# Kernel optimization log

Measured on AMD Instinct MI355X. Metric: run time of the kernel, lower is better.

The kernel has to match this reference:

```python
import jax, jax.numpy as jnp
import numpy as np

B, T, D, H = 2, 2048, 1024, 16
DK = D // H


def setup_inputs() -> dict:
    key = jax.random.key(0)
    ks = jax.random.split(key, 12)
    s = 0.02
    return {
        "query": jax.random.normal(ks[0], (B, T, D), jnp.float32),
        "key": jax.random.normal(ks[1], (B, T, D), jnp.float32),
        "value": jax.random.normal(ks[2], (B, T, D), jnp.float32),
        "mask": jax.random.randint(ks[3], (B, T), 0, 2) != 0,  # True = keep
        "Wq": jax.random.normal(ks[4], (D, D), jnp.float32) * s,
        "bq": jnp.zeros((D,), jnp.float32),
        "Wk": jax.random.normal(ks[5], (D, D), jnp.float32) * s,
        "bk": jnp.zeros((D,), jnp.float32),
        "Wv": jax.random.normal(ks[6], (D, D), jnp.float32) * s,
        "bv": jnp.zeros((D,), jnp.float32),
        "Wo": jax.random.normal(ks[7], (D, D), jnp.float32) * s,
        "bo": jnp.zeros((D,), jnp.float32),
    }


def _split_heads(x):
    # [B, S, D] -> [B, H, S, DK]
    b, s, _ = x.shape
    return x.reshape(b, s, H, DK).transpose(0, 2, 1, 3)


def reference(query, key, value, mask, Wq, bq, Wk, bk, Wv, bv, Wo, bo):
    # torch Linear: y = x @ W.T + b
    q = _split_heads(query @ Wq.T + bq)   # [B,H,T,DK]
    k = _split_heads(key @ Wk.T + bk)     # [B,H,S,DK]
    v = _split_heads(value @ Wv.T + bv)   # [B,H,S,DK]
    scale = 1.0 / np.sqrt(DK).astype(np.float32)
    scores = jnp.einsum('bhtd,bhsd->bhts', q, k) * scale  # [B,H,T,S]
    # key-padding mask [B,S] -> broadcast [B,1,1,S], True = keep
    scores = jnp.where(mask[:, None, None, :], scores, -jnp.inf)
    attn = jax.nn.softmax(scores, axis=-1)
    out = jnp.einsum('bhts,bhsd->bhtd', attn, v)           # [B,H,T,DK]
    out = out.transpose(0, 2, 1, 3).reshape(query.shape[0], -1, D)
    return out @ Wo.T + bo
```

## Files before the change

### kernel.cpp

```cpp
#include <hip/hip_runtime.h>
#include <stdint.h>

#define B_SZ 2
#define T_SEQ 2048
#define DMODEL 1024
#define NHEAD 16
#define DKH 64
#define M_ROWS (B_SZ * T_SEQ)

#define LDT 72

#define INP_E  4194304u
#define W_E    1048576u

typedef __bf16 bf16x8 __attribute__((ext_vector_type(8)));
typedef float  f32x4  __attribute__((ext_vector_type(4)));

__device__ __forceinline__ unsigned short f2bf(float f) {
    unsigned u = __builtin_bit_cast(unsigned, f);
    u += 0x7fffu + ((u >> 16) & 1u);
    return (unsigned short)(u >> 16);
}
__device__ __forceinline__ uint4 cvt8(const float* p) {
    float4 f0 = *(const float4*)p, f1 = *(const float4*)(p + 4);
    uint4 r;
    r.x = (unsigned)f2bf(f0.x) | ((unsigned)f2bf(f0.y) << 16);
    r.y = (unsigned)f2bf(f0.z) | ((unsigned)f2bf(f0.w) << 16);
    r.z = (unsigned)f2bf(f1.x) | ((unsigned)f2bf(f1.y) << 16);
    r.w = (unsigned)f2bf(f1.z) | ((unsigned)f2bf(f1.w) << 16);
    return r;
}

__device__ __forceinline__ void async16(const unsigned short* g, unsigned short* l) {
    __builtin_amdgcn_global_load_lds(
        (const __attribute__((address_space(1))) void*)g,
        (__attribute__((address_space(3))) void*)l, 16, 0, 0);
}

__global__ __launch_bounds__(256) void cvt_all(
    const float* __restrict__ q, const float* __restrict__ k, const float* __restrict__ v,
    const float* __restrict__ wq, const float* __restrict__ wk,
    const float* __restrict__ wv, const float* __restrict__ wo,
    unsigned short* __restrict__ wsb)
{
    int blk = blockIdx.x;
    const float* src; unsigned short* dst; int lb;
    if      (blk < 2048) { src = q;  dst = wsb;                       lb = blk; }
    else if (blk < 4096) { src = k;  dst = wsb + INP_E;               lb = blk - 2048; }
    else if (blk < 6144) { src = v;  dst = wsb + 2 * INP_E;           lb = blk - 4096; }
    else if (blk < 6656) { src = wq; dst = wsb + 3 * INP_E;           lb = blk - 6144; }
    else if (blk < 7168) { src = wk; dst = wsb + 3 * INP_E + W_E;     lb = blk - 6656; }
    else if (blk < 7680) { src = wv; dst = wsb + 3 * INP_E + 2 * W_E; lb = blk - 7168; }
    else                 { src = wo; dst = wsb + 3 * INP_E + 3 * W_E; lb = blk - 7680; }
    size_t i = ((size_t)lb * 256 + threadIdx.x) * 8;
    *(uint4*)&dst[i] = cvt8(src + i);
}

template<int C_MODE, int MT>
__device__ __forceinline__ void gemm_core(
    const unsigned short* __restrict__ A, const unsigned short* __restrict__ W,
    const float* __restrict__ bias, void* __restrict__ C,
    int N, int K, int bx, int by,
    unsigned short* sA, unsigned short* sB)
{
    const int tid  = threadIdx.x;
    const int wave = tid >> 6, lane = tid & 63;
    const int quad = lane >> 4, l15 = lane & 15;
    const int TM = MT * 32;
    const int m0 = by * TM, n0 = bx * 128;
    const int wm = (wave & 1) * (MT * 16), wn = (wave >> 1) * 64;

    f32x4 acc[MT][4] = {};

    for (int k0 = 0; k0 < K; k0 += 64) {
        __syncthreads();
        #pragma unroll
        for (int i = 0; i < MT; i++) {
            int c   = tid + 256 * i;
            int row = c >> 3;
            int gk  = ((c & 7) ^ (row & 7)) * 8;
            int sb  = (wave * 64 + 256 * i) * 8;
            async16(&A[(size_t)(m0 + row) * K + k0 + gk], sA + sb);
        }
        #pragma unroll
        for (int i = 0; i < 4; i++) {
            int c   = tid + 256 * i;
            int row = c >> 3;
            int gk  = ((c & 7) ^ (row & 7)) * 8;
            int sb  = (wave * 64 + 256 * i) * 8;
            async16(&W[(size_t)(n0 + row) * K + k0 + gk], sB + sb);
        }
        __syncthreads();
        const int sw = l15 & 7;
        #pragma unroll
        for (int ks = 0; ks < 2; ks++) {
            bf16x8 af[MT], bfv[4];
            #pragma unroll
            for (int mt = 0; mt < MT; mt++)
                af[mt] = *(const bf16x8*)&sA[(wm + mt * 16 + l15) * 64 +
                                             (((ks * 4 + quad) ^ sw) * 8)];
            #pragma unroll
            for (int nt = 0; nt < 4; nt++)
                bfv[nt] = *(const bf16x8*)&sB[(wn + nt * 16 + l15) * 64 +
                                              (((ks * 4 + quad) ^ sw) * 8)];
            #pragma unroll
            for (int mt = 0; mt < MT; mt++)
                #pragma unroll
                for (int nt = 0; nt < 4; nt++)
                    acc[mt][nt] = __builtin_amdgcn_mfma_f32_16x16x32_bf16(
                        af[mt], bfv[nt], acc[mt][nt], 0, 0, 0);
        }
    }

    if (C_MODE == 2) {
        #pragma unroll
        for (int mt = 0; mt < MT; mt++) {
            #pragma unroll
            for (int r = 0; r < 4; r++) {
                int m = m0 + wm + mt * 16 + quad * 4 + r;
                float bm = bias[m];
                #pragma unroll
                for (int nt = 0; nt < 4; nt++) {
                    int n = n0 + wn + nt * 16 + l15;
                    int bb = n >> 11, t = n & 2047;
                    ((unsigned short*)C)[((size_t)bb * 1024 + m) * 2048 + t] =
                        f2bf(acc[mt][nt][r] + bm);
                }
            }
        }
    } else {
        #pragma unroll
        for (int nt = 0; nt < 4; nt++) {
            int n = n0 + wn + nt * 16 + l15;
            float bv = bias[n];
            #pragma unroll
            for (int mt = 0; mt < MT; mt++) {
                #pragma unroll
                for (int r = 0; r < 4; r++) {
                    int m = m0 + wm + mt * 16 + quad * 4 + r;
                    float val = acc[mt][nt][r] + bv;
                    if (C_MODE == 1) ((float*)C)[(size_t)m * N + n] = val;
                    else ((unsigned short*)C)[(size_t)m * N + n] = f2bf(val);
                }
            }
        }
    }
}

__global__ __launch_bounds__(256) void gemm_qkv(
    const unsigned short* __restrict__ Qb, const unsigned short* __restrict__ Kb,
    const unsigned short* __restrict__ Vb,
    const unsigned short* __restrict__ Wqb, const unsigned short* __restrict__ Wkb,
    const unsigned short* __restrict__ Wvb,
    const float* __restrict__ bq, const float* __restrict__ bk, const float* __restrict__ bv,
    unsigned short* __restrict__ Qp, unsigned short* __restrict__ Kp,
    unsigned short* __restrict__ Vt)
{
    __shared__ __align__(16) unsigned short sA[128 * 64];
    __shared__ __align__(16) unsigned short sB[128 * 64];
    const int z = blockIdx.z, id = blockIdx.x;
    if (z < 2) {
        gemm_core<0, 4>(z ? Kb : Qb, z ? Wkb : Wqb, z ? bk : bq, z ? Kp : Qp,
                        DMODEL, DMODEL, id & 7, id >> 3, sA, sB);
    } else {
        gemm_core<2, 4>(Wvb, Vb, bv, Vt, M_ROWS, DMODEL, id & 31, id >> 5, sA, sB);
    }
}

__global__ __launch_bounds__(256) void gemm_o(
    const unsigned short* __restrict__ AO, const unsigned short* __restrict__ Wob,
    const float* __restrict__ bo, float* __restrict__ out)
{
    __shared__ __align__(16) unsigned short sA[64 * 64];
    __shared__ __align__(16) unsigned short sB[128 * 64];
    const int id = blockIdx.x;
    gemm_core<1, 2>(AO, Wob, bo, out, DMODEL, DMODEL, id & 7, id >> 3, sA, sB);
}

#define QBLK 128
#define KVB 64

__global__ __launch_bounds__(512) void attn_kernel(
    const unsigned short* __restrict__ Qp,
    const unsigned short* __restrict__ Kp,
    const unsigned short* __restrict__ Vt,
    const int* __restrict__ maskp,
    unsigned short* __restrict__ Op)
{
    __shared__ __align__(16) unsigned short sK[2][KVB * 64];
    __shared__ __align__(16) unsigned short sV[2][KVB * 64];
    __shared__ __align__(16) unsigned short sP[8 * 16 * LDT];
    __shared__ float smf[T_SEQ];

    const int tid  = threadIdx.x;
    const int wave = tid >> 6, lane = tid & 63;
    const int quad = lane >> 4, l15 = lane & 15;
    const int qblk = blockIdx.x, h = blockIdx.y, b = blockIdx.z;

    const float SCL2 = 0.125f * 1.44269504089f;
    const float MNEG = -30000.f;

    const int qrow = qblk * QBLK + wave * 16 + l15;
    const unsigned short* qptr = Qp + (size_t)(b * T_SEQ + qrow) * DMODEL + h * DKH + quad * 8;
    const bf16x8 aq0 = *(const bf16x8*)qptr;
    const bf16x8 aq1 = *(const bf16x8*)(qptr + 32);

    const unsigned short* Kb_ = Kp + (size_t)b * T_SEQ * DMODEL + h * DKH;
    const unsigned short* VtB = Vt + ((size_t)b * DMODEL + h * DKH) * T_SEQ;

    const int src_ = tid;
    const int srow = src_ >> 3;
    const int sgk  = ((src_ & 7) ^ (srow & 7)) * 8;
    const int ssb  = wave * 512;

    f32x4 O[4] = {};
    float l_r[4] = {0.f, 0.f, 0.f, 0.f};
    unsigned short* sPw = sP + wave * 16 * LDT;

    async16(&Kb_[(size_t)srow * DMODEL + sgk], &sK[0][ssb]);
    async16(&VtB[(size_t)srow * T_SEQ + sgk], &sV[0][ssb]);
    #pragma unroll
    for (int j = 0; j < 4; j++) {
        int i = tid + 512 * j;
        smf[i] = maskp[b * T_SEQ + i] ? 0.f : MNEG;
    }
    __syncthreads();

    const int sw = l15 & 7;
    for (int t = 0; t < T_SEQ / KVB; ++t) {
        const int cur = t & 1;
        const int s0 = t * KVB;
        if (t + 1 < T_SEQ / KVB) {
            async16(&Kb_[(size_t)(s0 + KVB + srow) * DMODEL + sgk], &sK[cur ^ 1][ssb]);
            async16(&VtB[(size_t)srow * T_SEQ + s0 + KVB + sgk], &sV[cur ^ 1][ssb]);
        }

        f32x4 S[4];
        __builtin_amdgcn_s_setprio(1);
        #pragma unroll
        for (int nt = 0; nt < 4; nt++) {
            const unsigned short* kr = &sK[cur][(nt * 16 + l15) * 64];
            f32x4 z = {};
            z = __builtin_amdgcn_mfma_f32_16x16x32_bf16(
                aq0, *(const bf16x8*)&kr[(quad ^ sw) * 8], z, 0, 0, 0);
            z = __builtin_amdgcn_mfma_f32_16x16x32_bf16(
                aq1, *(const bf16x8*)&kr[((quad + 4) ^ sw) * 8], z, 0, 0, 0);
            S[nt] = z;
        }
        __builtin_amdgcn_s_setprio(0);

        #pragma unroll
        for (int nt = 0; nt < 4; nt++) {
            float madd = smf[s0 + nt * 16 + l15];
            #pragma unroll
            for (int r = 0; r < 4; r++) {
                float p = __builtin_amdgcn_exp2f(fmaf(S[nt][r], SCL2, madd));
                l_r[r] += p;
                unsigned u = __builtin_bit_cast(unsigned, p) + 0x8000u;
                sPw[(quad * 4 + r) * LDT + nt * 16 + l15] = (unsigned short)(u >> 16);
            }
        }

        const bf16x8 ap0 = *(const bf16x8*)&sPw[l15 * LDT + quad * 8];
        const bf16x8 ap1 = *(const bf16x8*)&sPw[l15 * LDT + 32 + quad * 8];
        __builtin_amdgcn_s_setprio(1);
        #pragma unroll
        for (int nt = 0; nt < 4; nt++) {
            const unsigned short* vr = &sV[cur][(nt * 16 + l15) * 64];
            O[nt] = __builtin_amdgcn_mfma_f32_16x16x32_bf16(
                ap0, *(const bf16x8*)&vr[(quad ^ sw) * 8], O[nt], 0, 0, 0);
            O[nt] = __builtin_amdgcn_mfma_f32_16x16x32_bf16(
                ap1, *(const bf16x8*)&vr[((quad + 4) ^ sw) * 8], O[nt], 0, 0, 0);
        }
        __builtin_amdgcn_s_setprio(0);

        __syncthreads();
    }

    #pragma unroll
    for (int r = 0; r < 4; r++) {
        float l = l_r[r];
        l += __shfl_xor(l, 1);
        l += __shfl_xor(l, 2);
        l += __shfl_xor(l, 4);
        l += __shfl_xor(l, 8);
        l_r[r] = 1.0f / fmaxf(l, 1e-30f);
    }
    #pragma unroll
    for (int nt = 0; nt < 4; nt++) {
        #pragma unroll
        for (int r = 0; r < 4; r++) {
            int q = qblk * QBLK + wave * 16 + quad * 4 + r;
            Op[(size_t)(b * T_SEQ + q) * DMODEL + h * DKH + nt * 16 + l15] =
                f2bf(O[nt][r] * l_r[r]);
        }
    }
}

template<int A_BF16, int W_BF16, int C_MODE>
__global__ __launch_bounds__(256) void gemm_bt_cvt(
    const void* __restrict__ A_, const void* __restrict__ W_,
    const float* __restrict__ bias, void* __restrict__ C_,
    int M, int N, int K)
{
    __shared__ __align__(16) unsigned short sA[128 * LDT];
    __shared__ __align__(16) unsigned short sB[128 * LDT];
    const int tid  = threadIdx.x;
    const int wave = tid >> 6, lane = tid & 63;
    const int quad = lane >> 4, l15 = lane & 15;
    const int m0 = blockIdx.y * 128, n0 = blockIdx.x * 128;
    const int wm = (wave & 1) * 64, wn = (wave >> 1) * 64;
    f32x4 acc[4][4] = {};
    for (int k0 = 0; k0 < K; k0 += 64) {
        __syncthreads();
        #pragma unroll
        for (int i = 0; i < 4; i++) {
            int c = tid + 256 * i;
            int row = c >> 3, koff = (c & 7) * 8;
            if (A_BF16)
                *(uint4*)&sA[row * LDT + koff] =
                    *(const uint4*)&((const unsigned short*)A_)[(size_t)(m0 + row) * K + k0 + koff];
            else
                *(uint4*)&sA[row * LDT + koff] =
                    cvt8((const float*)A_ + (size_t)(m0 + row) * K + k0 + koff);
            if (W_BF16)
                *(uint4*)&sB[row * LDT + koff] =
                    *(const uint4*)&((const unsigned short*)W_)[(size_t)(n0 + row) * K + k0 + koff];
            else
                *(uint4*)&sB[row * LDT + koff] =
                    cvt8((const float*)W_ + (size_t)(n0 + row) * K + k0 + koff);
        }
        __syncthreads();
        #pragma unroll
        for (int ks = 0; ks < 2; ks++) {
            bf16x8 af[4], bfr[4];
            #pragma unroll
            for (int mt = 0; mt < 4; mt++)
                af[mt] = *(const bf16x8*)&sA[(wm + mt * 16 + l15) * LDT + ks * 32 + quad * 8];
            #pragma unroll
            for (int nt = 0; nt < 4; nt++)
                bfr[nt] = *(const bf16x8*)&sB[(wn + nt * 16 + l15) * LDT + ks * 32 + quad * 8];
            #pragma unroll
            for (int mt = 0; mt < 4; mt++)
                #pragma unroll
                for (int nt = 0; nt < 4; nt++)
                    acc[mt][nt] = __builtin_amdgcn_mfma_f32_16x16x32_bf16(
                        af[mt], bfr[nt], acc[mt][nt], 0, 0, 0);
        }
    }
    if (C_MODE == 2) {
        #pragma unroll
        for (int mt = 0; mt < 4; mt++)
            #pragma unroll
            for (int r = 0; r < 4; r++) {
                int m = m0 + wm + mt * 16 + quad * 4 + r;
                float bm = bias[m];
                #pragma unroll
                for (int nt = 0; nt < 4; nt++) {
                    int n = n0 + wn + nt * 16 + l15;
                    int bb = n >> 11, t = n & 2047;
                    ((unsigned short*)C_)[((size_t)bb * 1024 + m) * 2048 + t] =
                        f2bf(acc[mt][nt][r] + bm);
                }
            }
    } else {
        #pragma unroll
        for (int nt = 0; nt < 4; nt++) {
            int n = n0 + wn + nt * 16 + l15;
            float bv = bias[n];
            #pragma unroll
            for (int mt = 0; mt < 4; mt++)
                #pragma unroll
                for (int r = 0; r < 4; r++) {
                    int m = m0 + wm + mt * 16 + quad * 4 + r;
                    float val = acc[mt][nt][r] + bv;
                    if (C_MODE == 1) ((float*)C_)[(size_t)m * N + n] = val;
                    else ((unsigned short*)C_)[(size_t)m * N + n] = f2bf(val);
                }
        }
    }
}

extern "C" void kernel_launch(void* const* d_in, const int* in_sizes, int n_in,
                              void* d_out, int out_size, void* d_ws, size_t ws_size,
                              hipStream_t stream)
{
    const float* q  = (const float*)d_in[0];
    const float* k  = (const float*)d_in[1];
    const float* v  = (const float*)d_in[2];
    const int*   mk = (const int*)d_in[3];
    const float* Wq = (const float*)d_in[4];
    const float* bq = (const float*)d_in[5];
    const float* Wk = (const float*)d_in[6];
    const float* bk = (const float*)d_in[7];
    const float* Wv = (const float*)d_in[8];
    const float* bv = (const float*)d_in[9];
    const float* Wo = (const float*)d_in[10];
    const float* bo = (const float*)d_in[11];
    float* out = (float*)d_out;

    unsigned short* wsb = (unsigned short*)d_ws;
    const dim3 gA(T_SEQ / QBLK, NHEAD, B_SZ);

    if (ws_size >= (size_t)64 * 1024 * 1024) {
        unsigned short* Qb  = wsb;
        unsigned short* Kb  = wsb + INP_E;
        unsigned short* Vb  = wsb + 2 * INP_E;
        unsigned short* Wqb = wsb + 3 * INP_E;
        unsigned short* Wkb = wsb + 3 * INP_E + W_E;
        unsigned short* Wvb = wsb + 3 * INP_E + 2 * W_E;
        unsigned short* Wob = wsb + 3 * INP_E + 3 * W_E;
        unsigned short* Qp  = wsb + 4 * INP_E;
        unsigned short* Kp  = wsb + 5 * INP_E;
        unsigned short* Vt  = wsb + 6 * INP_E;
        unsigned short* AO  = wsb + 7 * INP_E;

        cvt_all<<<8192, 256, 0, stream>>>(q, k, v, Wq, Wk, Wv, Wo, wsb);
        gemm_qkv<<<dim3(256, 1, 3), 256, 0, stream>>>(
            Qb, Kb, Vb, Wqb, Wkb, Wvb, bq, bk, bv, Qp, Kp, Vt);
        attn_kernel<<<gA, 512, 0, stream>>>(Qp, Kp, Vt, mk, AO);
        gemm_o<<<dim3(512, 1, 1), 256, 0, stream>>>(AO, Wob, bo, out);
    } else {
        unsigned short* Qp = wsb;
        unsigned short* Kp = wsb + INP_E;
        unsigned short* Vt = wsb + 2 * INP_E;
        unsigned short* AO = wsb + 3 * INP_E;
        const dim3 gN(DMODEL / 128, M_ROWS / 128);
        const dim3 gV(M_ROWS / 128, DMODEL / 128);
        gemm_bt_cvt<0, 0, 0><<<gN, 256, 0, stream>>>(q, Wq, bq, Qp, M_ROWS, DMODEL, DMODEL);
        gemm_bt_cvt<0, 0, 0><<<gN, 256, 0, stream>>>(k, Wk, bk, Kp, M_ROWS, DMODEL, DMODEL);
        gemm_bt_cvt<0, 0, 2><<<gV, 256, 0, stream>>>(Wv, v, bv, Vt, DMODEL, M_ROWS, DMODEL);
        attn_kernel<<<gA, 512, 0, stream>>>(Qp, Kp, Vt, mk, AO);
        gemm_bt_cvt<1, 0, 1><<<gN, 256, 0, stream>>>(AO, Wo, bo, out, M_ROWS, DMODEL, DMODEL);
    }
}
```

Before: 234.6 us.

## Use 4 waves per attention block, each handling two 16-row query tiles

```diff
diff --git a/kernel.cpp b/kernel.cpp
--- a/kernel.cpp
+++ b/kernel.cpp
@@ -179,8 +179,9 @@
 
 #define QBLK 128
 #define KVB 64
-
-__global__ __launch_bounds__(512) void attn_kernel(
+#define AW 4
+
+__global__ __launch_bounds__(256) void attn_kernel(
     const unsigned short* __restrict__ Qp,
     const unsigned short* __restrict__ Kp,
     const unsigned short* __restrict__ Vt,
@@ -189,7 +190,7 @@
 {
     __shared__ __align__(16) unsigned short sK[2][KVB * 64];
     __shared__ __align__(16) unsigned short sV[2][KVB * 64];
-    __shared__ __align__(16) unsigned short sP[8 * 16 * LDT];
+    __shared__ __align__(16) unsigned short sP[AW * 32 * LDT];
     __shared__ float smf[T_SEQ];
 
     const int tid  = threadIdx.x;
@@ -200,28 +201,35 @@
     const float SCL2 = 0.125f * 1.44269504089f;
     const float MNEG = -30000.f;
 
-    const int qrow = qblk * QBLK + wave * 16 + l15;
-    const unsigned short* qptr = Qp + (size_t)(b * T_SEQ + qrow) * DMODEL + h * DKH + quad * 8;
-    const bf16x8 aq0 = *(const bf16x8*)qptr;
-    const bf16x8 aq1 = *(const bf16x8*)(qptr + 32);
+    bf16x8 aq[2][2];
+    #pragma unroll
+    for (int mt = 0; mt < 2; mt++) {
+        const int qrow = qblk * QBLK + wave * 32 + mt * 16 + l15;
+        const unsigned short* qptr =
+            Qp + (size_t)(b * T_SEQ + qrow) * DMODEL + h * DKH + quad * 8;
+        aq[mt][0] = *(const bf16x8*)qptr;
+        aq[mt][1] = *(const bf16x8*)(qptr + 32);
+    }
 
     const unsigned short* Kb_ = Kp + (size_t)b * T_SEQ * DMODEL + h * DKH;
     const unsigned short* VtB = Vt + ((size_t)b * DMODEL + h * DKH) * T_SEQ;
 
-    const int src_ = tid;
-    const int srow = src_ >> 3;
-    const int sgk  = ((src_ & 7) ^ (srow & 7)) * 8;
-    const int ssb  = wave * 512;
-
-    f32x4 O[4] = {};
-    float l_r[4] = {0.f, 0.f, 0.f, 0.f};
-    unsigned short* sPw = sP + wave * 16 * LDT;
-
-    async16(&Kb_[(size_t)srow * DMODEL + sgk], &sK[0][ssb]);
-    async16(&VtB[(size_t)srow * T_SEQ + sgk], &sV[0][ssb]);
+    f32x4 O[2][4] = {};
+    float l_r[2][4] = {};
+    unsigned short* sPw = sP + wave * 32 * LDT;
+
     #pragma unroll
-    for (int j = 0; j < 4; j++) {
-        int i = tid + 512 * j;
+    for (int i = 0; i < 2; i++) {
+        int c   = tid + 256 * i;
+        int row = c >> 3;
+        int gk  = ((c & 7) ^ (row & 7)) * 8;
+        int sb  = (wave * 64 + 256 * i) * 8;
+        async16(&Kb_[(size_t)row * DMODEL + gk], &sK[0][sb]);
+        async16(&VtB[(size_t)row * T_SEQ + gk], &sV[0][sb]);
+    }
+    #pragma unroll
+    for (int j = 0; j < 8; j++) {
+        int i = tid + 256 * j;
         smf[i] = maskp[b * T_SEQ + i] ? 0.f : MNEG;
     }
     __syncthreads();
@@ -231,68 +239,84 @@
         const int cur = t & 1;
         const int s0 = t * KVB;
         if (t + 1 < T_SEQ / KVB) {
-            async16(&Kb_[(size_t)(s0 + KVB + srow) * DMODEL + sgk], &sK[cur ^ 1][ssb]);
-            async16(&VtB[(size_t)srow * T_SEQ + s0 + KVB + sgk], &sV[cur ^ 1][ssb]);
-        }
-
-        f32x4 S[4];
-        __builtin_amdgcn_s_setprio(1);
+            #pragma unroll
+            for (int i = 0; i < 2; i++) {
+                int c   = tid + 256 * i;
+                int row = c >> 3;
+                int gk  = ((c & 7) ^ (row & 7)) * 8;
+                int sb  = (wave * 64 + 256 * i) * 8;
+                async16(&Kb_[(size_t)(s0 + KVB + row) * DMODEL + gk], &sK[cur ^ 1][sb]);
+                async16(&VtB[(size_t)row * T_SEQ + s0 + KVB + gk], &sV[cur ^ 1][sb]);
+            }
+        }
+
+        #pragma unroll
+        for (int mt = 0; mt < 2; mt++) {
+            f32x4 S[4];
+            __builtin_amdgcn_s_setprio(1);
+            #pragma unroll
+            for (int nt = 0; nt < 4; nt++) {
+                const unsigned short* kr = &sK[cur][(nt * 16 + l15) * 64];
+                f32x4 z = {};
+                z = __builtin_amdgcn_mfma_f32_16x16x32_bf16(
+                    aq[mt][0], *(const bf16x8*)&kr[(quad ^ sw) * 8], z, 0, 0, 0);
+                z = __builtin_amdgcn_mfma_f32_16x16x32_bf16(
+                    aq[mt][1], *(const bf16x8*)&kr[((quad + 4) ^ sw) * 8], z, 0, 0, 0);
+                S[nt] = z;
+            }
+            __builtin_amdgcn_s_setprio(0);
+            #pragma unroll
+            for (int nt = 0; nt < 4; nt++) {
+                float madd = smf[s0 + nt * 16 + l15];
+                #pragma unroll
+                for (int r = 0; r < 4; r++) {
+                    float p = __builtin_amdgcn_exp2f(fmaf(S[nt][r], SCL2, madd));
+                    l_r[mt][r] += p;
+                    unsigned u = __builtin_bit_cast(unsigned, p) + 0x8000u;
+                    sPw[(mt * 16 + quad * 4 + r) * LDT + nt * 16 + l15] =
+                        (unsigned short)(u >> 16);
+                }
+            }
+        }
+
+        #pragma unroll
+        for (int mt = 0; mt < 2; mt++) {
+            const bf16x8 ap0 = *(const bf16x8*)&sPw[(mt * 16 + l15) * LDT + quad * 8];
+            const bf16x8 ap1 = *(const bf16x8*)&sPw[(mt * 16 + l15) * LDT + 32 + quad * 8];
+            __builtin_amdgcn_s_setprio(1);
+            #pragma unroll
+            for (int nt = 0; nt < 4; nt++) {
+                const unsigned short* vr = &sV[cur][(nt * 16 + l15) * 64];
+                O[mt][nt] = __builtin_amdgcn_mfma_f32_16x16x32_bf16(
+                    ap0, *(const bf16x8*)&vr[(quad ^ sw) * 8], O[mt][nt], 0, 0, 0);
+                O[mt][nt] = __builtin_amdgcn_mfma_f32_16x16x32_bf16(
+                    ap1, *(const bf16x8*)&vr[((quad + 4) ^ sw) * 8], O[mt][nt], 0, 0, 0);
+            }
+            __builtin_amdgcn_s_setprio(0);
+        }
+
+        __syncthreads();
+    }
+
+    #pragma unroll
+    for (int mt = 0; mt < 2; mt++) {
+        #pragma unroll
+        for (int r = 0; r < 4; r++) {
+            float l = l_r[mt][r];
+            l += __shfl_xor(l, 1);
+            l += __shfl_xor(l, 2);
+            l += __shfl_xor(l, 4);
+            l += __shfl_xor(l, 8);
+            l_r[mt][r] = 1.0f / fmaxf(l, 1e-30f);
+        }
         #pragma unroll
         for (int nt = 0; nt < 4; nt++) {
-            const unsigned short* kr = &sK[cur][(nt * 16 + l15) * 64];
-            f32x4 z = {};
-            z = __builtin_amdgcn_mfma_f32_16x16x32_bf16(
-                aq0, *(const bf16x8*)&kr[(quad ^ sw) * 8], z, 0, 0, 0);
-            z = __builtin_amdgcn_mfma_f32_16x16x32_bf16(
-                aq1, *(const bf16x8*)&kr[((quad + 4) ^ sw) * 8], z, 0, 0, 0);
-            S[nt] = z;
-        }
-        __builtin_amdgcn_s_setprio(0);
-
-        #pragma unroll
-        for (int nt = 0; nt < 4; nt++) {
-            float madd = smf[s0 + nt * 16 + l15];
             #pragma unroll
             for (int r = 0; r < 4; r++) {
-                float p = __builtin_amdgcn_exp2f(fmaf(S[nt][r], SCL2, madd));
-                l_r[r] += p;
-                unsigned u = __builtin_bit_cast(unsigned, p) + 0x8000u;
-                sPw[(quad * 4 + r) * LDT + nt * 16 + l15] = (unsigned short)(u >> 16);
-            }
-        }
-
-        const bf16x8 ap0 = *(const bf16x8*)&sPw[l15 * LDT + quad * 8];
-        const bf16x8 ap1 = *(const bf16x8*)&sPw[l15 * LDT + 32 + quad * 8];
-        __builtin_amdgcn_s_setprio(1);
-        #pragma unroll
-        for (int nt = 0; nt < 4; nt++) {
-            const unsigned short* vr = &sV[cur][(nt * 16 + l15) * 64];
-            O[nt] = __builtin_amdgcn_mfma_f32_16x16x32_bf16(
-                ap0, *(const bf16x8*)&vr[(quad ^ sw) * 8], O[nt], 0, 0, 0);
-            O[nt] = __builtin_amdgcn_mfma_f32_16x16x32_bf16(
-                ap1, *(const bf16x8*)&vr[((quad + 4) ^ sw) * 8], O[nt], 0, 0, 0);
-        }
-        __builtin_amdgcn_s_setprio(0);
-
-        __syncthreads();
-    }
-
-    #pragma unroll
-    for (int r = 0; r < 4; r++) {
-        float l = l_r[r];
-        l += __shfl_xor(l, 1);
-        l += __shfl_xor(l, 2);
-        l += __shfl_xor(l, 4);
-        l += __shfl_xor(l, 8);
-        l_r[r] = 1.0f / fmaxf(l, 1e-30f);
-    }
-    #pragma unroll
-    for (int nt = 0; nt < 4; nt++) {
-        #pragma unroll
-        for (int r = 0; r < 4; r++) {
-            int q = qblk * QBLK + wave * 16 + quad * 4 + r;
-            Op[(size_t)(b * T_SEQ + q) * DMODEL + h * DKH + nt * 16 + l15] =
-                f2bf(O[nt][r] * l_r[r]);
+                int q = qblk * QBLK + wave * 32 + mt * 16 + quad * 4 + r;
+                Op[(size_t)(b * T_SEQ + q) * DMODEL + h * DKH + nt * 16 + l15] =
+                    f2bf(O[mt][nt][r] * l_r[mt][r]);
+            }
         }
     }
 }
@@ -418,7 +442,7 @@
         cvt_all<<<8192, 256, 0, stream>>>(q, k, v, Wq, Wk, Wv, Wo, wsb);
         gemm_qkv<<<dim3(256, 1, 3), 256, 0, stream>>>(
             Qb, Kb, Vb, Wqb, Wkb, Wvb, bq, bk, bv, Qp, Kp, Vt);
-        attn_kernel<<<gA, 512, 0, stream>>>(Qp, Kp, Vt, mk, AO);
+        attn_kernel<<<gA, 256, 0, stream>>>(Qp, Kp, Vt, mk, AO);
         gemm_o<<<dim3(512, 1, 1), 256, 0, stream>>>(AO, Wob, bo, out);
     } else {
         unsigned short* Qp = wsb;
@@ -430,7 +454,7 @@
         gemm_bt_cvt<0, 0, 0><<<gN, 256, 0, stream>>>(q, Wq, bq, Qp, M_ROWS, DMODEL, DMODEL);
         gemm_bt_cvt<0, 0, 0><<<gN, 256, 0, stream>>>(k, Wk, bk, Kp, M_ROWS, DMODEL, DMODEL);
         gemm_bt_cvt<0, 0, 2><<<gV, 256, 0, stream>>>(Wv, v, bv, Vt, DMODEL, M_ROWS, DMODEL);
-        attn_kernel<<<gA, 512, 0, stream>>>(Qp, Kp, Vt, mk, AO);
+        attn_kernel<<<gA, 256, 0, stream>>>(Qp, Kp, Vt, mk, AO);
         gemm_bt_cvt<1, 0, 1><<<gN, 256, 0, stream>>>(AO, Wo, bo, out, M_ROWS, DMODEL, DMODEL);
     }
 }
```

After: 248.2 us. +5.8%, slower.
